# Kernel optimization log

Hardware: AMD Instinct MI355X
Metric: run time of the kernel (lower is better)

The kernel has to match this reference:

```python
import jax, jax.numpy as jnp
import numpy as np

N, M, B, L, C, H = 4096, 16384, 8, 96, 512, 8
Dh = C // H


def setup_inputs() -> dict:
    key0 = jax.random.key(0)
    ks = jax.random.split(key0, 8)
    query = jax.random.normal(ks[0], (N, C), dtype=jnp.float32)
    key_t = jax.random.normal(ks[1], (M, C), dtype=jnp.float32)
    value = jax.random.normal(ks[2], (M, C), dtype=jnp.float32)
    keys_per_batch = M // B  # 2048 local key indices per scene
    idx = jax.random.randint(ks[3], (N, L), 0, keys_per_batch)
    pad = jax.random.uniform(ks[4], (N, L)) < 0.1
    pad = pad.at[:, 0].set(False)
    index_pair = jnp.where(pad, -1, idx).astype(jnp.int64)
    query_batch_cnt = jnp.full((B,), N // B, dtype=jnp.int32)
    key_batch_cnt = jnp.full((B,), M // B, dtype=jnp.int32)
    index_pair_batch = jnp.repeat(jnp.arange(B, dtype=jnp.int64), N // B)
    in_proj_weight = jax.random.normal(ks[5], (3 * C, C), dtype=jnp.float32) * (1.0 / np.sqrt(C))
    in_proj_bias = jnp.zeros((3 * C,), dtype=jnp.float32)
    out_proj_weight = jax.random.normal(ks[6], (C, C), dtype=jnp.float32) * (1.0 / np.sqrt(C))
    out_proj_bias = jnp.zeros((C,), dtype=jnp.float32)
    return {
        "query": query, "key": key_t, "value": value,
        "index_pair": index_pair, "query_batch_cnt": query_batch_cnt,
        "key_batch_cnt": key_batch_cnt, "index_pair_batch": index_pair_batch,
        "in_proj_weight": in_proj_weight, "in_proj_bias": in_proj_bias,
        "out_proj_weight": out_proj_weight, "out_proj_bias": out_proj_bias,
    }


def reference(query, key, value, index_pair, query_batch_cnt, key_batch_cnt,
              index_pair_batch, in_proj_weight, in_proj_bias,
              out_proj_weight, out_proj_bias):
    n, c = query.shape
    l = index_pair.shape[1]
    scaling = float(Dh) ** -0.5
    # QKV projections (F.linear: x @ W.T + b)
    q = query @ in_proj_weight[:c].T + in_proj_bias[:c]
    k = key @ in_proj_weight[c:2 * c].T + in_proj_bias[c:2 * c]
    v = value @ in_proj_weight[2 * c:].T + in_proj_bias[2 * c:]
    q = (q * scaling).reshape(n, H, Dh)
    k = k.reshape(-1, H, Dh)
    v = v.reshape(-1, H, Dh)
    mask = index_pair < 0  # (N, L)
    # convert local per-batch key index to global index via exclusive cumsum of key counts
    offs = jnp.concatenate([jnp.zeros((1,), key_batch_cnt.dtype), jnp.cumsum(key_batch_cnt)[:-1]])
    gidx = jnp.where(mask, 0, index_pair + offs[index_pair_batch][:, None])  # (N, L)
    k_g = k[gidx]  # (N, L, H, Dh)
    attn = jnp.einsum('nhd,nlhd->nlh', q, k_g)
    attn = jnp.where(mask[:, :, None], -jnp.inf, attn)
    attn = jax.nn.softmax(attn, axis=1)  # softmax over neighbor dim L
    v_g = v[gidx]  # (N, L, H, Dh)
    out = jnp.einsum('nlh,nlhd->nhd', attn, v_g).reshape(n, c)
    out = out @ out_proj_weight.T + out_proj_bias
    return out, attn.sum(axis=-1) / H
```

## Files before the change

kernel.cpp:

```cpp
#include <hip/hip_runtime.h>
#include <hip/hip_fp16.h>
#include <cstdint>
#include <cstddef>

#define N_Q 4096
#define M_K 16384
#define LNB 96
#define CH  512
#define NH  8

typedef _Float16 half8  __attribute__((ext_vector_type(8)));
typedef _Float16 h2     __attribute__((ext_vector_type(2)));
typedef float    floatx4 __attribute__((ext_vector_type(4)));
typedef float    floatx2 __attribute__((ext_vector_type(2)));

union H8 { half8 v; h2 p[4]; };

__device__ __forceinline__ h2 cvt2(float a, float b) {
    return __builtin_bit_cast(h2, __builtin_amdgcn_cvt_pkrtz(a, b));
}

__device__ __forceinline__ void async16(const void* g, void* l) {
    __builtin_amdgcn_global_load_lds(
        (const __attribute__((address_space(1))) void*)g,
        (__attribute__((address_space(3))) void*)l, 16, 0, 0);
}

template<int CTRL>
__device__ __forceinline__ float dpp_addf(float x) {
    int xi = __builtin_bit_cast(int, x);
    int yi = __builtin_amdgcn_update_dpp(xi, xi, CTRL, 0xF, 0xF, false);
    return x + __builtin_bit_cast(float, yi);
}
__device__ __forceinline__ float octet_sum(float x) {
    x = dpp_addf<0x141>(x);
    x = dpp_addf<0x4E>(x);
    x = dpp_addf<0xB1>(x);
    return x;
}

__global__ void cvt_weights(const float* __restrict__ wIn, const float* __restrict__ wOut,
                            _Float16* __restrict__ dst) {
    const size_t i = (size_t)blockIdx.x * blockDim.x + threadIdx.x;
    const float4 v = (i < 196608) ? ((const float4*)wIn)[i]
                                  : ((const float4*)wOut)[i - 196608];
    h2 a = cvt2(v.x, v.y);
    h2 b = cvt2(v.z, v.w);
    *(h2*)&dst[i * 4]     = a;
    *(h2*)&dst[i * 4 + 2] = b;
}

template<int OUTF16, int TM, int AFP32>
__device__ __forceinline__ void gemm_body(
    const void* __restrict__ Ap, const _Float16* __restrict__ Bw,
    const float* __restrict__ bias, void* __restrict__ outp, float oscale,
    int bm, int bn)
{
    constexpr int MI = TM / 32;
    __shared__ alignas(16) _Float16 As[TM * 32];
    __shared__ alignas(16) _Float16 Bs[128 * 32];

    const int t    = threadIdx.x;
    const int lane = t & 63;
    const int wave = t >> 6;
    const int wm   = wave >> 1, wn = wave & 1;

    floatx4 acc[MI][4] = {};

    const int rowL = t >> 2;
    const int kcol = (t & 3) * 8;
    const _Float16* gB = Bw + (size_t)(bn * 128 + rowL) * CH + kcol;
    _Float16* lB = &Bs[rowL * 32 + kcol];

    const _Float16* gA16 = nullptr; _Float16* lA16 = nullptr;
    const float* gA32 = nullptr; _Float16* lA32 = nullptr;
    if constexpr (AFP32) {
        gA32 = (const float*)Ap + (size_t)(bm * TM + rowL) * CH + kcol;
        lA32 = &As[rowL * 32 + kcol];
    } else {
        gA16 = (const _Float16*)Ap + (size_t)(bm * TM + rowL) * CH + kcol;
        lA16 = &As[rowL * 32 + kcol];
    }

    const int r0 = lane & 15;
    const int ko = (lane >> 4) * 8;

    for (int kt = 0; kt < CH / 32; ++kt) {
        if constexpr (AFP32) {
            const float* ga = gA32 + kt * 32;
            float4 x0 = ((const float4*)ga)[0], x1 = ((const float4*)ga)[1];
            H8 o0;
            o0.p[0] = cvt2(x0.x, x0.y);
            o0.p[1] = cvt2(x0.z, x0.w);
            o0.p[2] = cvt2(x1.x, x1.y);
            o0.p[3] = cvt2(x1.z, x1.w);
            *(half8*)lA32 = o0.v;
        } else {
            const _Float16* a0 = gA16 + kt * 32;
            async16(a0, lA16);
        }
        const _Float16* b0 = gB + kt * 32;
        async16(b0,           lB);
        async16(b0 + 64 * CH, lB + 64 * 32);
        __syncthreads();

        half8 af[MI], bf[4];
        #pragma unroll
        for (int mi = 0; mi < MI; ++mi)
            af[mi] = *(const half8*)&As[(wm * (TM / 2) + mi * 16 + r0) * 32 + ko];
        #pragma unroll
        for (int ni = 0; ni < 4; ++ni)
            bf[ni] = *(const half8*)&Bs[(wn * 64 + ni * 16 + r0) * 32 + ko];
        #pragma unroll
        for (int mi = 0; mi < MI; ++mi)
            #pragma unroll
            for (int ni = 0; ni < 4; ++ni)
                acc[mi][ni] = __builtin_amdgcn_mfma_f32_16x16x32_f16(
                    af[mi], bf[ni], acc[mi][ni], 0, 0, 0);
        __syncthreads();
    }

    #pragma unroll
    for (int mi = 0; mi < MI; ++mi) {
        #pragma unroll
        for (int ni = 0; ni < 4; ++ni) {
            const int col = bn * 128 + wn * 64 + ni * 16 + (lane & 15);
            const float bv = bias[col];
            #pragma unroll
            for (int r = 0; r < 4; ++r) {
                const int row = bm * TM + wm * (TM / 2) + mi * 16 + (lane >> 4) * 4 + r;
                const float v = (acc[mi][ni][r] + bv) * oscale;
                if (OUTF16) ((_Float16*)outp)[(size_t)row * CH + col] = (_Float16)v;
                else        ((float*)outp)[(size_t)row * CH + col]    = v;
            }
        }
    }
}

template<int OUTF16, int TM, int AFP32>
__global__ __launch_bounds__(256) void gemm_k(
    const void* __restrict__ A, const _Float16* __restrict__ Bw,
    const float* __restrict__ bias, void* __restrict__ outp, float oscale)
{
    const int bid = blockIdx.x;
    const int x   = bid & 7;
    const int i   = bid >> 3;
    const int bn  = i & 3;
    const int bm  = x + 8 * (i >> 2);
    gemm_body<OUTF16, TM, AFP32>(A, Bw, bias, outp, oscale, bm, bn);
}

#define KV_STAGE(AS, BS, KT) do {                                               \
    _Pragma("unroll")                                                           \
    for (int q = 0; q < 4; ++q)                                                 \
        async16(Ab + aoff[q] + (KT) * 128, (char*)(AS) + (q * 256 + t) * 16);   \
    _Pragma("unroll")                                                           \
    for (int q = 0; q < 2; ++q)                                                 \
        async16(Bb + boff[q] + (KT) * 64,  (char*)(BS) + (q * 256 + t) * 16);   \
    __builtin_amdgcn_sched_barrier(0);                                          \
} while (0)

#define KV_COMPUTE(AS, BS) do {                                                 \
    half8 af[4], bf[4];                                                         \
    _Pragma("unroll")                                                           \
    for (int mi = 0; mi < 4; ++mi) {                                            \
        const int row = wm * 64 + mi * 16 + r0;                                 \
        const float4 x0 = *(const float4*)((const char*)(AS) + row * 128 + (((hi * 2)     ^ swz) * 16)); \
        const float4 x1 = *(const float4*)((const char*)(AS) + row * 128 + (((hi * 2 + 1) ^ swz) * 16)); \
        H8 o;                                                                   \
        o.p[0] = cvt2(x0.x, x0.y);                                              \
        o.p[1] = cvt2(x0.z, x0.w);                                              \
        o.p[2] = cvt2(x1.x, x1.y);                                              \
        o.p[3] = cvt2(x1.z, x1.w);                                              \
        af[mi] = o.v;                                                           \
    }                                                                           \
    _Pragma("unroll")                                                           \
    for (int ni = 0; ni < 4; ++ni) {                                            \
        const int row   = wn * 64 + ni * 16 + r0;                               \
        const int super = row >> 1;                                             \
        const int vv    = ((row & 1) * 4 + hi) ^ (super & 7);                   \
        bf[ni] = *(const half8*)((const char*)(BS) + super * 128 + vv * 16);    \
    }                                                                           \
    _Pragma("unroll")                                                           \
    for (int mi = 0; mi < 4; ++mi)                                              \
        _Pragma("unroll")                                                       \
        for (int ni = 0; ni < 4; ++ni)                                          \
            acc[mi][ni] = __builtin_amdgcn_mfma_f32_16x16x32_f16(               \
                af[mi], bf[ni], acc[mi][ni], 0, 0, 0);                          \
} while (0)

#define KV_SYNC() do {                                                          \
    asm volatile("s_waitcnt vmcnt(0)" ::: "memory");                            \
    __builtin_amdgcn_s_barrier();                                               \
    __builtin_amdgcn_sched_barrier(0);                                          \
} while (0)

__global__ __launch_bounds__(256) void gemm_kv(
    const float* __restrict__ keyp, const float* __restrict__ valp,
    const _Float16* __restrict__ w16, const float* __restrict__ bIn,
    _Float16* __restrict__ k16, _Float16* __restrict__ v16)
{
    const int bid = blockIdx.x;
    const int x   = bid & 7;
    const int i   = bid >> 3;
    const int bn  = i & 3;
    const int z   = (i >> 2) & 1;
    const int bm  = x + 8 * (i >> 3);

    const char*     Ab   = (const char*)(z ? valp : keyp);
    const char*     Bb   = (const char*)(w16 + (size_t)(z ? 1024 : 512) * 512);
    const float*    bias = bIn + (z ? 1024 : 512);
    _Float16*       outp = z ? v16 : k16;

    __shared__ alignas(16) float    As0[128 * 32];
    __shared__ alignas(16) float    As1[128 * 32];
    __shared__ alignas(16) _Float16 Bs0[128 * 32];
    __shared__ alignas(16) _Float16 Bs1[128 * 32];

    const int t    = threadIdx.x;
    const int lane = t & 63;
    const int wave = t >> 6;
    const int wm   = wave >> 1, wn = wave & 1;

    floatx4 acc[4][4] = {};

    uint32_t aoff[4];
    #pragma unroll
    for (int q = 0; q < 4; ++q) {
        const int G   = q * 256 + t;
        const int row = G >> 3;
        const int g   = (G & 7) ^ (row & 7);
        aoff[q] = (uint32_t)((bm * 128 + row) * 2048 + g * 16);
    }
    uint32_t boff[2];
    #pragma unroll
    for (int q = 0; q < 2; ++q) {
        const int G     = q * 256 + t;
        const int super = G >> 3;
        const int sgg   = (G & 7) ^ (super & 7);
        const int row   = super * 2 + (sgg >> 2);
        const int g     = sgg & 3;
        boff[q] = (uint32_t)((bn * 128 + row) * 1024 + g * 16);
    }

    const int r0  = lane & 15;
    const int hi  = lane >> 4;
    const int swz = r0 & 7;

    KV_STAGE(As0, Bs0, 0);
    KV_SYNC();

    #pragma unroll 1
    for (int ktp = 0; ktp < 8; ++ktp) {
        const int kt0 = ktp * 2;
        KV_STAGE(As1, Bs1, kt0 + 1);
        KV_COMPUTE(As0, Bs0);
        KV_SYNC();
        if (kt0 + 2 < 16) KV_STAGE(As0, Bs0, kt0 + 2);
        KV_COMPUTE(As1, Bs1);
        if (ktp < 7) KV_SYNC();
    }

    #pragma unroll
    for (int mi = 0; mi < 4; ++mi) {
        #pragma unroll
        for (int ni = 0; ni < 4; ++ni) {
            const int col = bn * 128 + wn * 64 + ni * 16 + (lane & 15);
            const float bv = bias[col];
            #pragma unroll
            for (int r = 0; r < 4; ++r) {
                const int row = bm * 128 + wm * 64 + mi * 16 + (lane >> 4) * 4 + r;
                outp[(size_t)row * CH + col] = (_Float16)(acc[mi][ni][r] + bv);
            }
        }
    }
}

__global__ __launch_bounds__(256) void attn_kernel(
    const _Float16* __restrict__ q16, const _Float16* __restrict__ k16,
    const _Float16* __restrict__ v16, const int* __restrict__ ipair,
    const int* __restrict__ ibatch, const int* __restrict__ kcnt,
    _Float16* __restrict__ op16, float* __restrict__ aout)
{
    __shared__ uint32_t vmask[LNB];
    __shared__ float    pls[LNB * 9];
    __shared__ __half2  pph[LNB * 9];
    __shared__ float    part[4][CH];

    const int t = threadIdx.x;
    const int n = ((blockIdx.x & 7) << 9) | (blockIdx.x >> 3);

    if (t < LNB) {
        const int idx = ipair[(size_t)n * LNB + t];
        const int b   = ibatch[n];
        int off = 0;
        for (int i = 0; i < b; ++i) off += kcnt[i];
        const uint32_t vo = (uint32_t)((idx < 0 ? 0 : (idx + off)) * (CH * 2));
        vmask[t] = vo | (idx < 0 ? 0x80000000u : 0u);
    }
    __syncthreads();

    const int lane = t & 63, wv = t >> 6;
    const int h    = lane >> 3;
    const int l0   = wv * 24;

    {
        const half8 qv = *(const half8*)(q16 + (size_t)n * CH + lane * 8);
        H8 qu; qu.v = qv;
        const char* kbase = (const char*)k16 + lane * 16;
        const int4* vb = (const int4*)&vmask[l0];
        for (int g = 0; g < 3; ++g) {
            const int4 w0 = vb[2 * g], w1 = vb[2 * g + 1];
            uint32_t vm8[8] = {(uint32_t)w0.x, (uint32_t)w0.y, (uint32_t)w0.z, (uint32_t)w0.w,
                               (uint32_t)w1.x, (uint32_t)w1.y, (uint32_t)w1.z, (uint32_t)w1.w};
            #pragma unroll
            for (int j = 0; j < 8; ++j) {
                const uint32_t vms = __builtin_amdgcn_readfirstlane(vm8[j]);
                H8 ku; ku.v = *(const half8*)(kbase + (vms & 0x7fffffffu));
                float acc = 0.f;
                #pragma unroll
                for (int u = 0; u < 4; ++u)
                    acc = __builtin_amdgcn_fdot2(qu.p[u], ku.p[u], acc, false);
                acc = octet_sum(acc);
                if ((lane & 7) == 0)
                    pls[(l0 + g * 8 + j) * 9 + h] = (vms & 0x80000000u) ? -1e30f : acc;
            }
        }
    }
    __syncthreads();

    {
        const int hh = t >> 5, j = t & 31;
        const float v0 = pls[j * 9 + hh];
        const float v1 = pls[(j + 32) * 9 + hh];
        const float v2 = pls[(j + 64) * 9 + hh];
        float m = fmaxf(v0, fmaxf(v1, v2));
        #pragma unroll
        for (int s = 16; s >= 1; s >>= 1) m = fmaxf(m, __shfl_xor(m, s, 32));
        const float e0 = __expf(v0 - m), e1 = __expf(v1 - m), e2 = __expf(v2 - m);
        float ssum = e0 + e1 + e2;
        #pragma unroll
        for (int s = 16; s >= 1; s >>= 1) ssum += __shfl_xor(ssum, s, 32);
        const float rinv = 1.0f / ssum;
        const float p0 = e0 * rinv, p1 = e1 * rinv, p2 = e2 * rinv;
        pls[j * 9 + hh]        = p0;
        pls[(j + 32) * 9 + hh] = p1;
        pls[(j + 64) * 9 + hh] = p2;
        pph[j * 9 + hh]        = __half2half2(__float2half_rn(p0));
        pph[(j + 32) * 9 + hh] = __half2half2(__float2half_rn(p1));
        pph[(j + 64) * 9 + hh] = __half2half2(__float2half_rn(p2));
    }
    __syncthreads();

    if (t < LNB) {
        float s = 0.f;
        #pragma unroll
        for (int u = 0; u < NH; ++u) s += pls[t * 9 + u];
        aout[(size_t)n * LNB + t] = s * (1.0f / NH);
    }

    {
        float accf[8] = {};
        const char* vbase = (const char*)v16 + lane * 16;
        const int4* vb = (const int4*)&vmask[l0];
        const __half2 hz = __half2half2(__float2half_rn(0.f));
        for (int g = 0; g < 3; ++g) {
            const int4 w0 = vb[2 * g], w1 = vb[2 * g + 1];
            uint32_t vm8[8] = {(uint32_t)w0.x, (uint32_t)w0.y, (uint32_t)w0.z, (uint32_t)w0.w,
                               (uint32_t)w1.x, (uint32_t)w1.y, (uint32_t)w1.z, (uint32_t)w1.w};
            __half2 a0 = hz, a1 = hz, a2 = hz, a3 = hz;
            #pragma unroll
            for (int j = 0; j < 8; ++j) {
                const uint32_t vms = __builtin_amdgcn_readfirstlane(vm8[j]);
                const half8 vv = *(const half8*)(vbase + (vms & 0x7fffffffu));
                union { half8 v; __half2 q[4]; } vu; vu.v = vv;
                const __half2 pp = pph[(l0 + g * 8 + j) * 9 + h];
                a0 = __hfma2(pp, vu.q[0], a0);
                a1 = __hfma2(pp, vu.q[1], a1);
                a2 = __hfma2(pp, vu.q[2], a2);
                a3 = __hfma2(pp, vu.q[3], a3);
            }
            float2 f;
            f = __half22float2(a0); accf[0] += f.x; accf[1] += f.y;
            f = __half22float2(a1); accf[2] += f.x; accf[3] += f.y;
            f = __half22float2(a2); accf[4] += f.x; accf[5] += f.y;
            f = __half22float2(a3); accf[6] += f.x; accf[7] += f.y;
        }
        floatx4 lo, hi;
        #pragma unroll
        for (int u = 0; u < 4; ++u) { lo[u] = accf[u]; hi[u] = accf[u + 4]; }
        *(floatx4*)&part[wv][lane * 8]     = lo;
        *(floatx4*)&part[wv][lane * 8 + 4] = hi;
    }
    __syncthreads();

    {
        const int c = t * 2;
        floatx2 s = *(const floatx2*)&part[0][c];
        #pragma unroll
        for (int w = 1; w < 4; ++w) {
            floatx2 pw = *(const floatx2*)&part[w][c];
            s[0] += pw[0]; s[1] += pw[1];
        }
        h2 o; o[0] = (_Float16)s[0]; o[1] = (_Float16)s[1];
        *(h2*)&op16[(size_t)n * CH + c] = o;
    }
}

extern "C" void kernel_launch(void* const* d_in, const int* in_sizes, int n_in,
                              void* d_out, int out_size, void* d_ws, size_t ws_size,
                              hipStream_t stream)
{
    const float* query = (const float*)d_in[0];
    const float* key   = (const float*)d_in[1];
    const float* value = (const float*)d_in[2];
    const int*   ipair = (const int*)d_in[3];
    const int*   kcnt  = (const int*)d_in[5];
    const int*   ibat  = (const int*)d_in[6];
    const float* wIn   = (const float*)d_in[7];
    const float* bIn   = (const float*)d_in[8];
    const float* wOut  = (const float*)d_in[9];
    const float* bOut  = (const float*)d_in[10];

    float* out  = (float*)d_out;
    float* aout = out + (size_t)N_Q * CH;

    char* ws = (char*)d_ws;
    _Float16* w16  = (_Float16*)(ws);
    _Float16* wo16 = (_Float16*)(ws + 1572864);
    _Float16* q16  = (_Float16*)(ws + 2097152);
    _Float16* k16  = (_Float16*)(ws + 6291456);
    _Float16* v16  = (_Float16*)(ws + 23068672);
    _Float16* op16 = (_Float16*)(ws + 39845888);

    cvt_weights<<<1024, 256, 0, stream>>>(wIn, wOut, w16);

    gemm_k<1, 64, 1><<<256, 256, 0, stream>>>(query, w16, bIn, q16, 0.125f);

    gemm_kv<<<1024, 256, 0, stream>>>(key, value, w16, bIn, k16, v16);

    attn_kernel<<<4096, 256, 0, stream>>>(q16, k16, v16, ipair, ibat, kcnt, op16, aout);

    gemm_k<0, 64, 0><<<256, 256, 0, stream>>>(op16, wo16, bOut, d_out, 1.0f);
}
```

Before: 99.94 us.

## Load fp32 A operand directly into registers in KV projection GEMM

Replaces the async global-to-LDS staging of the fp32 key/value activations with direct per-thread float4 global loads into registers, double-buffered across k-tiles, and keeps only the fp16 weight tile in LDS. This removes the LDS footprint and LDS reads for A and allows three blocks per CU via launch bounds. It trades this for more register pressure and uncoalesced-ish row-strided global loads with no cross-wave reuse of A, and it relies on __syncthreads rather than explicit vmcnt waits for the async B loads.

```diff
diff --git a/kernel.cpp b/kernel.cpp
--- a/kernel.cpp
+++ b/kernel.cpp
@@ -150,28 +150,28 @@
     gemm_body<OUTF16, TM, AFP32>(A, Bw, bias, outp, oscale, bm, bn);
 }
 
-#define KV_STAGE(AS, BS, KT) do {                                               \
-    _Pragma("unroll")                                                           \
-    for (int q = 0; q < 4; ++q)                                                 \
-        async16(Ab + aoff[q] + (KT) * 128, (char*)(AS) + (q * 256 + t) * 16);   \
+#define KV_LOAD_A(DST, KT) do {                                                 \
+    DST[0][0] = gA0[(KT) * 8];     DST[0][1] = gA0[(KT) * 8 + 1];               \
+    DST[1][0] = gA1[(KT) * 8];     DST[1][1] = gA1[(KT) * 8 + 1];               \
+    DST[2][0] = gA2[(KT) * 8];     DST[2][1] = gA2[(KT) * 8 + 1];               \
+    DST[3][0] = gA3[(KT) * 8];     DST[3][1] = gA3[(KT) * 8 + 1];               \
+} while (0)
+
+#define KV_STAGE_B(BS, KT) do {                                                 \
     _Pragma("unroll")                                                           \
     for (int q = 0; q < 2; ++q)                                                 \
-        async16(Bb + boff[q] + (KT) * 64,  (char*)(BS) + (q * 256 + t) * 16);   \
-    __builtin_amdgcn_sched_barrier(0);                                          \
+        async16(Bb + boff[q] + (KT) * 64, (char*)(BS) + (q * 256 + t) * 16);    \
 } while (0)
 
-#define KV_COMPUTE(AS, BS) do {                                                 \
+#define KV_MFMA(ASRC, BS) do {                                                  \
     half8 af[4], bf[4];                                                         \
     _Pragma("unroll")                                                           \
     for (int mi = 0; mi < 4; ++mi) {                                            \
-        const int row = wm * 64 + mi * 16 + r0;                                 \
-        const float4 x0 = *(const float4*)((const char*)(AS) + row * 128 + (((hi * 2)     ^ swz) * 16)); \
-        const float4 x1 = *(const float4*)((const char*)(AS) + row * 128 + (((hi * 2 + 1) ^ swz) * 16)); \
         H8 o;                                                                   \
-        o.p[0] = cvt2(x0.x, x0.y);                                              \
-        o.p[1] = cvt2(x0.z, x0.w);                                              \
-        o.p[2] = cvt2(x1.x, x1.y);                                              \
-        o.p[3] = cvt2(x1.z, x1.w);                                              \
+        o.p[0] = cvt2(ASRC[mi][0].x, ASRC[mi][0].y);                            \
+        o.p[1] = cvt2(ASRC[mi][0].z, ASRC[mi][0].w);                            \
+        o.p[2] = cvt2(ASRC[mi][1].x, ASRC[mi][1].y);                            \
+        o.p[3] = cvt2(ASRC[mi][1].z, ASRC[mi][1].w);                            \
         af[mi] = o.v;                                                           \
     }                                                                           \
     _Pragma("unroll")                                                           \
@@ -189,13 +189,7 @@
                 af[mi], bf[ni], acc[mi][ni], 0, 0, 0);                          \
 } while (0)
 
-#define KV_SYNC() do {                                                          \
-    asm volatile("s_waitcnt vmcnt(0)" ::: "memory");                            \
-    __builtin_amdgcn_s_barrier();                                               \
-    __builtin_amdgcn_sched_barrier(0);                                          \
-} while (0)
-
-__global__ __launch_bounds__(256) void gemm_kv(
+__global__ __launch_bounds__(256, 3) void gemm_kv(
     const float* __restrict__ keyp, const float* __restrict__ valp,
     const _Float16* __restrict__ w16, const float* __restrict__ bIn,
     _Float16* __restrict__ k16, _Float16* __restrict__ v16)
@@ -207,13 +201,11 @@
     const int z   = (i >> 2) & 1;
     const int bm  = x + 8 * (i >> 3);
 
-    const char*     Ab   = (const char*)(z ? valp : keyp);
+    const float*    Af   = z ? valp : keyp;
     const char*     Bb   = (const char*)(w16 + (size_t)(z ? 1024 : 512) * 512);
     const float*    bias = bIn + (z ? 1024 : 512);
     _Float16*       outp = z ? v16 : k16;
 
-    __shared__ alignas(16) float    As0[128 * 32];
-    __shared__ alignas(16) float    As1[128 * 32];
     __shared__ alignas(16) _Float16 Bs0[128 * 32];
     __shared__ alignas(16) _Float16 Bs1[128 * 32];
 
@@ -221,17 +213,17 @@
     const int lane = t & 63;
     const int wave = t >> 6;
     const int wm   = wave >> 1, wn = wave & 1;
+    const int r0   = lane & 15;
+    const int hi   = lane >> 4;
 
     floatx4 acc[4][4] = {};
 
-    uint32_t aoff[4];
-    #pragma unroll
-    for (int q = 0; q < 4; ++q) {
-        const int G   = q * 256 + t;
-        const int row = G >> 3;
-        const int g   = (G & 7) ^ (row & 7);
-        aoff[q] = (uint32_t)((bm * 128 + row) * 2048 + g * 16);
-    }
+    const int rowg = bm * 128 + wm * 64 + r0;
+    const float4* gA0 = (const float4*)(Af + (size_t)(rowg +  0) * CH) + hi * 2;
+    const float4* gA1 = (const float4*)(Af + (size_t)(rowg + 16) * CH) + hi * 2;
+    const float4* gA2 = (const float4*)(Af + (size_t)(rowg + 32) * CH) + hi * 2;
+    const float4* gA3 = (const float4*)(Af + (size_t)(rowg + 48) * CH) + hi * 2;
+
     uint32_t boff[2];
     #pragma unroll
     for (int q = 0; q < 2; ++q) {
@@ -243,23 +235,29 @@
         boff[q] = (uint32_t)((bn * 128 + row) * 1024 + g * 16);
     }
 
-    const int r0  = lane & 15;
-    const int hi  = lane >> 4;
-    const int swz = r0 & 7;
-
-    KV_STAGE(As0, Bs0, 0);
-    KV_SYNC();
+    float4 aC[4][2], aN[4][2];
+
+    KV_LOAD_A(aC, 0);
+    KV_STAGE_B(Bs0, 0);
+    __syncthreads();
 
     #pragma unroll 1
-    for (int ktp = 0; ktp < 8; ++ktp) {
-        const int kt0 = ktp * 2;
-        KV_STAGE(As1, Bs1, kt0 + 1);
-        KV_COMPUTE(As0, Bs0);
-        KV_SYNC();
-        if (kt0 + 2 < 16) KV_STAGE(As0, Bs0, kt0 + 2);
-        KV_COMPUTE(As1, Bs1);
-        if (ktp < 7) KV_SYNC();
-    }
+    for (int ktp = 0; ktp < 7; ++ktp) {
+        const int kt0 = 2 * ktp;
+        KV_LOAD_A(aN, kt0 + 1);
+        KV_STAGE_B(Bs1, kt0 + 1);
+        KV_MFMA(aC, Bs0);
+        __syncthreads();
+        KV_LOAD_A(aC, kt0 + 2);
+        KV_STAGE_B(Bs0, kt0 + 2);
+        KV_MFMA(aN, Bs1);
+        __syncthreads();
+    }
+    KV_LOAD_A(aN, 15);
+    KV_STAGE_B(Bs1, 15);
+    KV_MFMA(aC, Bs0);
+    __syncthreads();
+    KV_MFMA(aN, Bs1);
 
     #pragma unroll
     for (int mi = 0; mi < 4; ++mi) {
```

Measured after the change: 149.0 us. 49.1% more time.

## Merge Q and KV projections into one kernel with triple-buffered LDS pipeline

Applied to the files above, without the earlier changes.

Replaces the separate Q projection GEMM launch and the K/V GEMM with a single proj_qkv kernel of 1152 blocks. Blocks beyond 1024 handle the query projection with 128-row tiles and apply the scaling factor in the epilogue. The K-loop changes from double-buffered staging with full vmcnt(0) waits to a three-stage LDS ring using partial vmcnt waits, so global loads overlap more with MFMA work. This removes one launch and the tail gap between the two GEMMs. The cost is 72KB of LDS per block, which may lower occupancy.

```diff
diff --git a/kernel.cpp b/kernel.cpp
--- a/kernel.cpp
+++ b/kernel.cpp
@@ -150,23 +150,28 @@
     gemm_body<OUTF16, TM, AFP32>(A, Bw, bias, outp, oscale, bm, bn);
 }
 
-#define KV_STAGE(AS, BS, KT) do {                                               \
+#define PSTAGE(B, KT) do {                                                      \
     _Pragma("unroll")                                                           \
     for (int q = 0; q < 4; ++q)                                                 \
-        async16(Ab + aoff[q] + (KT) * 128, (char*)(AS) + (q * 256 + t) * 16);   \
+        async16(Ab + aoff[q] + (KT) * 128,                                      \
+                LdsA + (B) * 24576 + (q * 256 + t) * 16);                       \
     _Pragma("unroll")                                                           \
     for (int q = 0; q < 2; ++q)                                                 \
-        async16(Bb + boff[q] + (KT) * 64,  (char*)(BS) + (q * 256 + t) * 16);   \
+        async16(Bb + boff[q] + (KT) * 64,                                       \
+                LdsA + (B) * 24576 + 16384 + (q * 256 + t) * 16);               \
     __builtin_amdgcn_sched_barrier(0);                                          \
 } while (0)
 
-#define KV_COMPUTE(AS, BS) do {                                                 \
+#define PCOMPUTE(B) do {                                                        \
+    const char* As_ = LdsA + (B) * 24576;                                       \
+    const char* Bs_ = LdsA + (B) * 24576 + 16384;                               \
     half8 af[4], bf[4];                                                         \
     _Pragma("unroll")                                                           \
     for (int mi = 0; mi < 4; ++mi) {                                            \
         const int row = wm * 64 + mi * 16 + r0;                                 \
-        const float4 x0 = *(const float4*)((const char*)(AS) + row * 128 + (((hi * 2)     ^ swz) * 16)); \
-        const float4 x1 = *(const float4*)((const char*)(AS) + row * 128 + (((hi * 2 + 1) ^ swz) * 16)); \
+        const int swz = row & 7;                                                \
+        const float4 x0 = *(const float4*)(As_ + row * 128 + (((hi * 2)     ^ swz) * 16)); \
+        const float4 x1 = *(const float4*)(As_ + row * 128 + (((hi * 2 + 1) ^ swz) * 16)); \
         H8 o;                                                                   \
         o.p[0] = cvt2(x0.x, x0.y);                                              \
         o.p[1] = cvt2(x0.z, x0.w);                                              \
@@ -179,7 +184,7 @@
         const int row   = wn * 64 + ni * 16 + r0;                               \
         const int super = row >> 1;                                             \
         const int vv    = ((row & 1) * 4 + hi) ^ (super & 7);                   \
-        bf[ni] = *(const half8*)((const char*)(BS) + super * 128 + vv * 16);    \
+        bf[ni] = *(const half8*)(Bs_ + super * 128 + vv * 16);                  \
     }                                                                           \
     _Pragma("unroll")                                                           \
     for (int mi = 0; mi < 4; ++mi)                                              \
@@ -187,40 +192,63 @@
         for (int ni = 0; ni < 4; ++ni)                                          \
             acc[mi][ni] = __builtin_amdgcn_mfma_f32_16x16x32_f16(               \
                 af[mi], bf[ni], acc[mi][ni], 0, 0, 0);                          \
+    __builtin_amdgcn_sched_barrier(0);                                          \
 } while (0)
 
-#define KV_SYNC() do {                                                          \
-    asm volatile("s_waitcnt vmcnt(0)" ::: "memory");                            \
+#define PVW(N) do {                                                             \
+    asm volatile("s_waitcnt vmcnt(" #N ")" ::: "memory");                       \
+    __builtin_amdgcn_sched_barrier(0);                                          \
+} while (0)
+#define PBAR() do {                                                             \
     __builtin_amdgcn_s_barrier();                                               \
     __builtin_amdgcn_sched_barrier(0);                                          \
 } while (0)
 
-__global__ __launch_bounds__(256) void gemm_kv(
-    const float* __restrict__ keyp, const float* __restrict__ valp,
-    const _Float16* __restrict__ w16, const float* __restrict__ bIn,
+__global__ __launch_bounds__(256) void proj_qkv(
+    const float* __restrict__ query, const float* __restrict__ keyp,
+    const float* __restrict__ valp, const _Float16* __restrict__ w16,
+    const float* __restrict__ bIn, _Float16* __restrict__ q16,
     _Float16* __restrict__ k16, _Float16* __restrict__ v16)
 {
+    __shared__ alignas(16) char LdsA[73728];
+
     const int bid = blockIdx.x;
-    const int x   = bid & 7;
-    const int i   = bid >> 3;
-    const int bn  = i & 3;
-    const int z   = (i >> 2) & 1;
-    const int bm  = x + 8 * (i >> 3);
-
-    const char*     Ab   = (const char*)(z ? valp : keyp);
-    const char*     Bb   = (const char*)(w16 + (size_t)(z ? 1024 : 512) * 512);
-    const float*    bias = bIn + (z ? 1024 : 512);
-    _Float16*       outp = z ? v16 : k16;
-
-    __shared__ alignas(16) float    As0[128 * 32];
-    __shared__ alignas(16) float    As1[128 * 32];
-    __shared__ alignas(16) _Float16 Bs0[128 * 32];
-    __shared__ alignas(16) _Float16 Bs1[128 * 32];
+    const float* Af; const _Float16* W; const float* bias; _Float16* dst;
+    float osc; int bm, bn;
+
+    if (bid < 1024) {
+        const int x = bid & 7;
+        const int i = bid >> 3;
+        bn = i & 3;
+        const int z = (i >> 2) & 1;
+        bm = x + 8 * (i >> 3);
+        Af   = z ? valp : keyp;
+        W    = w16 + (size_t)(z ? 1024 : 512) * 512;
+        bias = bIn + (z ? 1024 : 512);
+        dst  = z ? v16 : k16;
+        osc  = 1.0f;
+    } else {
+        const int j = bid - 1024;
+        const int x = j & 7;
+        const int jj = j >> 3;
+        bn = jj & 3;
+        bm = x + 8 * (jj >> 2);
+        Af   = query;
+        W    = w16;
+        bias = bIn;
+        dst  = q16;
+        osc  = 0.125f;
+    }
+
+    const char* Ab = (const char*)Af;
+    const char* Bb = (const char*)W;
 
     const int t    = threadIdx.x;
     const int lane = t & 63;
     const int wave = t >> 6;
     const int wm   = wave >> 1, wn = wave & 1;
+    const int r0   = lane & 15;
+    const int hi   = lane >> 4;
 
     floatx4 acc[4][4] = {};
 
@@ -243,34 +271,47 @@
         boff[q] = (uint32_t)((bn * 128 + row) * 1024 + g * 16);
     }
 
-    const int r0  = lane & 15;
-    const int hi  = lane >> 4;
-    const int swz = r0 & 7;
-
-    KV_STAGE(As0, Bs0, 0);
-    KV_SYNC();
+    PSTAGE(0, 0);
+    PSTAGE(1, 1);
+    PSTAGE(2, 2);
 
     #pragma unroll 1
-    for (int ktp = 0; ktp < 8; ++ktp) {
-        const int kt0 = ktp * 2;
-        KV_STAGE(As1, Bs1, kt0 + 1);
-        KV_COMPUTE(As0, Bs0);
-        KV_SYNC();
-        if (kt0 + 2 < 16) KV_STAGE(As0, Bs0, kt0 + 2);
-        KV_COMPUTE(As1, Bs1);
-        if (ktp < 7) KV_SYNC();
-    }
+    for (int j = 0; j < 4; ++j) {
+        const int s = 3 * j;
+        PVW(12); PBAR();
+        PCOMPUTE(0);
+        PBAR();
+        PSTAGE(0, s + 3);
+        PVW(12); PBAR();
+        PCOMPUTE(1);
+        PBAR();
+        PSTAGE(1, s + 4);
+        PVW(12); PBAR();
+        PCOMPUTE(2);
+        PBAR();
+        PSTAGE(2, s + 5);
+    }
+    PVW(12); PBAR();
+    PCOMPUTE(0);
+    PBAR();
+    PSTAGE(0, 15);
+    PVW(12); PBAR();
+    PCOMPUTE(1);
+    PVW(6);  PBAR();
+    PCOMPUTE(2);
+    PVW(0);  PBAR();
+    PCOMPUTE(0);
 
     #pragma unroll
     for (int mi = 0; mi < 4; ++mi) {
         #pragma unroll
         for (int ni = 0; ni < 4; ++ni) {
-            const int col = bn * 128 + wn * 64 + ni * 16 + (lane & 15);
+            const int col = bn * 128 + wn * 64 + ni * 16 + r0;
             const float bv = bias[col];
             #pragma unroll
             for (int r = 0; r < 4; ++r) {
-                const int row = bm * 128 + wm * 64 + mi * 16 + (lane >> 4) * 4 + r;
-                outp[(size_t)row * CH + col] = (_Float16)(acc[mi][ni][r] + bv);
+                const int row = bm * 128 + wm * 64 + mi * 16 + hi * 4 + r;
+                dst[(size_t)row * CH + col] = (_Float16)((acc[mi][ni][r] + bv) * osc);
             }
         }
     }
@@ -435,9 +476,7 @@
 
     cvt_weights<<<1024, 256, 0, stream>>>(wIn, wOut, w16);
 
-    gemm_k<1, 64, 1><<<256, 256, 0, stream>>>(query, w16, bIn, q16, 0.125f);
-
-    gemm_kv<<<1024, 256, 0, stream>>>(key, value, w16, bIn, k16, v16);
+    proj_qkv<<<1152, 256, 0, stream>>>(query, key, value, w16, bIn, q16, k16, v16);
 
     attn_kernel<<<4096, 256, 0, stream>>>(q16, k16, v16, ipair, ibat, kcnt, op16, aout);
 
```

New measurement: 97.45 us (median of 2 runs). 2.5% less time.
